# Kernel tuning notes

Hardware: AMD Instinct MI355X
Metric: run time of the kernel (lower is better)

The kernel has to match this reference:

```python
import jax, jax.numpy as jnp
import numpy as np

EPS = 1e-6


def _phi(x):
    # feature map: ELU(x) + 1, strictly positive
    return jax.nn.elu(x) + 1.0


def setup_inputs() -> dict:
    key = jax.random.key(0)
    kq, kk, kv, km, kz = jax.random.split(key, 5)
    B, H, T, D = 2, 32, 4096, 128
    Q = jax.random.normal(kq, (B, H, T, D), dtype=jnp.float32)
    K = jax.random.normal(kk, (B, H, T, D), dtype=jnp.float32)
    V = jax.random.normal(kv, (B, H, T, D), dtype=jnp.float32)
    M = jax.random.normal(km, (H, D, D), dtype=jnp.float32)
    z = jax.random.uniform(kz, (H, D), dtype=jnp.float32)
    return {"Q": Q, "K": K, "V": V, "M": M, "z": z}


def reference(Q, K, V, M, z):
    # ---- retrieve(Q) ----
    phi_Q = _phi(Q)                                   # (b,h,t,d)
    retrieved = jnp.einsum('bhtd,hde->bhte', phi_Q, M)
    norm = jnp.einsum('bhtd,hd->bht', phi_Q, z)[..., None]
    out = retrieved / jnp.maximum(norm, EPS)          # (b,h,t,d)

    # ---- update(K, V): detached (stop_gradient) running accumulation ----
    phi_K_b = _phi(jax.lax.stop_gradient(K)).mean(0)  # (h,t,d)
    V_b = jax.lax.stop_gradient(V).mean(0)            # (h,t,d)
    M_new = M + jnp.einsum('htd,hte->hde', phi_K_b, V_b)
    z_new = z + phi_K_b.sum(1)
    return out, M_new, z_new
```

## Files before the change

### kernel.cpp

```cpp
#include <hip/hip_runtime.h>
#include <cstdint>
#include <cstddef>


typedef __bf16 bf16x8 __attribute__((ext_vector_type(8)));
typedef float  f32x4  __attribute__((ext_vector_type(4)));
typedef unsigned short us8v __attribute__((ext_vector_type(8)));

#define NB 2
#define NH 32
#define NT 4096
#define ND 128
#define NC 8
#define TCH (NT / NC)
#define NUPD (NH * NC)
#define NOUT (NB * NH * (NT / 128))
#define EPSF 1e-6f

__device__ __forceinline__ float phi_f(float x) {
    return x > 0.0f ? x + 1.0f : __expf(x);
}

__device__ __forceinline__ unsigned short f2bf(float f) {
    union { float f; unsigned u; } c; c.f = f;
    unsigned r = c.u + 0x7FFFu + ((c.u >> 16) & 1u);
    return (unsigned short)(r >> 16);
}

__device__ __forceinline__ bf16x8 pack8(float a0, float a1, float a2, float a3,
                                        float a4, float a5, float a6, float a7) {
    union { us8v u; bf16x8 h; } r;
    r.u[0] = f2bf(a0); r.u[1] = f2bf(a1); r.u[2] = f2bf(a2); r.u[3] = f2bf(a3);
    r.u[4] = f2bf(a4); r.u[5] = f2bf(a5); r.u[6] = f2bf(a6); r.u[7] = f2bf(a7);
    return r.h;
}

__global__ __launch_bounds__(256) void k_prep(const float* __restrict__ M,
                                              unsigned short* __restrict__ Mt) {
    int idx = blockIdx.x * 256 + threadIdx.x;
    int h = idx >> 14, rem = idx & 16383;
    int e = rem >> 7, d = rem & 127;
    Mt[idx] = f2bf(M[(h << 14) + (d << 7) + e]);
}

__device__ __forceinline__ void upd_body(int blk, const float* __restrict__ K,
                                         const float* __restrict__ V,
                                         float* __restrict__ part,
                                         float* __restrict__ zpart,
                                         unsigned short* smem, float* zacc) {
    const int tid = threadIdx.x;
    const int h = blk >> 3, ch = blk & 7;
    unsigned short* Kl = smem;
    unsigned short* Vl = smem + 8192;

    const size_t bstr = (size_t)NH * NT * ND;
    const float* K0 = K + (size_t)h * NT * ND + (size_t)ch * TCH * ND;
    const float* K1 = K0 + bstr;
    const float* V0 = V + (size_t)h * NT * ND + (size_t)ch * TCH * ND;
    const float* V1 = V0 + bstr;
    if (tid < 128) zacc[tid] = 0.0f;

    const int L = tid & 31, d0 = L << 2, tb = tid >> 5;
    const int lane = tid & 63, wave = tid >> 6;
    const int mw = (wave & 1) << 6, nw = (wave >> 1) << 6;
    const int l15 = lane & 15, qd = lane >> 4;
    const int grp = tb ^ (L & 7);

    float zp0 = 0.f, zp1 = 0.f, zp2 = 0.f, zp3 = 0.f;
    f32x4 acc[4][4];
#pragma unroll
    for (int a = 0; a < 4; ++a)
#pragma unroll
        for (int b = 0; b < 4; ++b) acc[a][b] = (f32x4){0.f, 0.f, 0.f, 0.f};

    for (int st = 0; st < TCH / 64; ++st) {
        us8v kpu[4], vpu[4];
#pragma unroll
        for (int i = 0; i < 8; ++i) {
            size_t off = ((size_t)(st * 64 + tb * 8 + i)) * ND + d0;
            float4 a0 = *(const float4*)(K0 + off);
            float4 a1 = *(const float4*)(K1 + off);
            float4 b0 = *(const float4*)(V0 + off);
            float4 b1 = *(const float4*)(V1 + off);
            float p0 = 0.5f * (phi_f(a0.x) + phi_f(a1.x));
            float p1 = 0.5f * (phi_f(a0.y) + phi_f(a1.y));
            float p2 = 0.5f * (phi_f(a0.z) + phi_f(a1.z));
            float p3 = 0.5f * (phi_f(a0.w) + phi_f(a1.w));
            zp0 += p0; zp1 += p1; zp2 += p2; zp3 += p3;
            kpu[0][i] = f2bf(p0); kpu[1][i] = f2bf(p1);
            kpu[2][i] = f2bf(p2); kpu[3][i] = f2bf(p3);
            vpu[0][i] = f2bf(0.5f * (b0.x + b1.x));
            vpu[1][i] = f2bf(0.5f * (b0.y + b1.y));
            vpu[2][i] = f2bf(0.5f * (b0.z + b1.z));
            vpu[3][i] = f2bf(0.5f * (b0.w + b1.w));
        }
        __syncthreads();
#pragma unroll
        for (int j = 0; j < 4; ++j) {
            *(us8v*)&Kl[(d0 + j) * 64 + grp * 8] = kpu[j];
            *(us8v*)&Vl[(d0 + j) * 64 + grp * 8] = vpu[j];
        }
        __syncthreads();
#pragma unroll
        for (int kk = 0; kk < 2; ++kk) {
            bf16x8 af[4], bv[4];
#pragma unroll
            for (int im = 0; im < 4; ++im) {
                int d = mw + im * 16 + l15;
                int sg = (kk * 4 + qd) ^ ((d >> 2) & 7);
                af[im] = *(const bf16x8*)&Kl[d * 64 + sg * 8];
            }
#pragma unroll
            for (int in = 0; in < 4; ++in) {
                int e = nw + in * 16 + l15;
                int sg = (kk * 4 + qd) ^ ((e >> 2) & 7);
                bv[in] = *(const bf16x8*)&Vl[e * 64 + sg * 8];
            }
#pragma unroll
            for (int im = 0; im < 4; ++im)
#pragma unroll
                for (int in = 0; in < 4; ++in)
                    acc[im][in] = __builtin_amdgcn_mfma_f32_16x16x32_bf16(
                        af[im], bv[in], acc[im][in], 0, 0, 0);
        }
    }

    atomicAdd(&zacc[d0 + 0], zp0);
    atomicAdd(&zacc[d0 + 1], zp1);
    atomicAdd(&zacc[d0 + 2], zp2);
    atomicAdd(&zacc[d0 + 3], zp3);
    __syncthreads();
    if (tid < 128) zpart[((size_t)h * NC + ch) * 128 + tid] = zacc[tid];

    float* pb = part + ((size_t)h * NC + ch) * 16384;
#pragma unroll
    for (int im = 0; im < 4; ++im)
#pragma unroll
        for (int in = 0; in < 4; ++in) {
            int col = nw + in * 16 + l15;
#pragma unroll
            for (int rg = 0; rg < 4; ++rg) {
                int row = mw + im * 16 + qd * 4 + rg;
                pb[(size_t)row * ND + col] = acc[im][in][rg];
            }
        }
}

__device__ __forceinline__ void out_body(int blk, const float* __restrict__ Q,
                                         const unsigned short* __restrict__ Mt,
                                         const float* __restrict__ z,
                                         float* __restrict__ out,
                                         unsigned short* smem) {
    const int tid = threadIdx.x;
    const int tile = blk & 31, bh = blk >> 5, h = bh & 31;
    const float* Qb = Q + ((size_t)bh * NT + (size_t)tile * 128) * ND;
    unsigned short* Bs = smem;

    {
        const us8v* src = (const us8v*)(Mt + (size_t)h * 16384);
#pragma unroll
        for (int i = 0; i < 8; ++i) {
            int idx = i * 256 + tid;
            int e = idx >> 4, d8 = idx & 15;
            *(us8v*)&Bs[e * 136 + d8 * 8] = src[idx];
        }
    }
    const int lane = tid & 63, wave = tid >> 6;
    const int mw = (wave & 1) << 6, nw = (wave >> 1) << 6;
    const int l15 = lane & 15, qd = lane >> 4;

    bf16x8 zf[4];
#pragma unroll
    for (int kk = 0; kk < 4; ++kk) {
        const float* zp = z + h * ND + kk * 32 + qd * 8;
        float4 z0 = *(const float4*)zp;
        float4 z1 = *(const float4*)(zp + 4);
        zf[kk] = pack8(z0.x, z0.y, z0.z, z0.w, z1.x, z1.y, z1.z, z1.w);
    }
    __syncthreads();

    f32x4 acc[4][4], accN[4];
#pragma unroll
    for (int a = 0; a < 4; ++a) {
        accN[a] = (f32x4){0.f, 0.f, 0.f, 0.f};
#pragma unroll
        for (int b = 0; b < 4; ++b) acc[a][b] = (f32x4){0.f, 0.f, 0.f, 0.f};
    }

#pragma unroll
    for (int im = 0; im < 4; ++im) {
        int row = mw + im * 16 + l15;
        const float* qr = Qb + (size_t)row * ND;
        bf16x8 af[4];
#pragma unroll
        for (int kk = 0; kk < 4; ++kk) {
            const float* qp = qr + kk * 32 + qd * 8;
            float4 q0 = *(const float4*)qp;
            float4 q1 = *(const float4*)(qp + 4);
            af[kk] = pack8(phi_f(q0.x), phi_f(q0.y), phi_f(q0.z), phi_f(q0.w),
                           phi_f(q1.x), phi_f(q1.y), phi_f(q1.z), phi_f(q1.w));
        }
#pragma unroll
        for (int kk = 0; kk < 4; ++kk)
            accN[im] = __builtin_amdgcn_mfma_f32_16x16x32_bf16(
                af[kk], zf[kk], accN[im], 0, 0, 0);
#pragma unroll
        for (int in = 0; in < 4; ++in) {
            int e = nw + in * 16 + l15;
#pragma unroll
            for (int kk = 0; kk < 4; ++kk) {
                bf16x8 bv = *(const bf16x8*)&Bs[e * 136 + kk * 32 + qd * 8];
                acc[im][in] = __builtin_amdgcn_mfma_f32_16x16x32_bf16(
                    af[kk], bv, acc[im][in], 0, 0, 0);
            }
        }
    }

    float* outb = out + ((size_t)bh * NT + (size_t)tile * 128) * ND;
#pragma unroll
    for (int im = 0; im < 4; ++im) {
#pragma unroll
        for (int rg = 0; rg < 4; ++rg) {
            float inv = 1.0f / fmaxf(accN[im][rg], EPSF);
            int row = mw + im * 16 + qd * 4 + rg;
#pragma unroll
            for (int in = 0; in < 4; ++in) {
                int col = nw + in * 16 + l15;
                outb[(size_t)row * ND + col] = acc[im][in][rg] * inv;
            }
        }
    }
}

__global__ __launch_bounds__(256) void k_main(const float* __restrict__ Q,
                                              const float* __restrict__ K,
                                              const float* __restrict__ V,
                                              const unsigned short* __restrict__ Mt,
                                              const float* __restrict__ z,
                                              float* __restrict__ out,
                                              float* __restrict__ part,
                                              float* __restrict__ zpart) {
    __shared__ unsigned short smem[128 * 136];
    __shared__ float zacc[128];
    if (blockIdx.x < NUPD)
        upd_body(blockIdx.x, K, V, part, zpart, smem, zacc);
    else
        out_body(blockIdx.x - NUPD, Q, Mt, z, out, smem);
}

__global__ __launch_bounds__(256) void k_reduce(const float* __restrict__ M,
                                                const float* __restrict__ z,
                                                const float* __restrict__ part,
                                                const float* __restrict__ zpart,
                                                float* __restrict__ outM,
                                                float* __restrict__ outz) {
    int idx = blockIdx.x * 256 + threadIdx.x;
    int h = idx >> 14, de = idx & 16383;
    float s = M[idx];
    const float* p = part + (size_t)h * NC * 16384 + de;
#pragma unroll
    for (int c = 0; c < NC; ++c) s += p[(size_t)c * 16384];
    outM[idx] = s;
    if (idx < NH * ND) {
        int hh = idx >> 7, d = idx & 127;
        float sz = z[idx];
        const float* pz = zpart + (size_t)hh * NC * 128 + d;
#pragma unroll
        for (int c = 0; c < NC; ++c) sz += pz[c * 128];
        outz[idx] = sz;
    }
}

extern "C" void kernel_launch(void* const* d_in, const int* in_sizes, int n_in,
                              void* d_out, int out_size, void* d_ws, size_t ws_size,
                              hipStream_t stream) {
    const float* Q = (const float*)d_in[0];
    const float* K = (const float*)d_in[1];
    const float* V = (const float*)d_in[2];
    const float* M = (const float*)d_in[3];
    const float* z = (const float*)d_in[4];

    float* out0 = (float*)d_out;
    float* outM = out0 + (size_t)NB * NH * NT * ND;
    float* outz = outM + (size_t)NH * ND * ND;

    unsigned short* Mt = (unsigned short*)d_ws;
    float* part  = (float*)((char*)d_ws + (1u << 20));
    float* zpart = part + (size_t)NH * NC * ND * ND;

    k_prep<<<2048, 256, 0, stream>>>(M, Mt);
    k_main<<<NUPD + NOUT, 256, 0, stream>>>(Q, K, V, Mt, z, out0, part, zpart);
    k_reduce<<<(NH * ND * ND) / 256, 256, 0, stream>>>(M, z, part, zpart, outM, outz);
}
```

Baseline: 424.0 us.

## Use native bf16 conversion, swizzled LDS, smaller shared memory and occupancy hint

Replaces the manual round-to-nearest-even bf16 packing with native __bf16 casts, which can map to hardware conversion instructions. Moves the 0.5 and 0.25 mean scales out of the inner loop and applies them at the partial-sum stores. Replaces the padded 136-stride LDS layout for M with an XOR-swizzled 128-stride layout and reuses that buffer for the z accumulator. Adds a launch_bounds hint of 4 blocks per CU and uses the hardware reciprocal for normalisation. The native casts and the fast reciprocal may round differently from the old code, and the occupancy hint may increase register spills.

```diff
diff --git a/kernel.cpp b/kernel.cpp
--- a/kernel.cpp
+++ b/kernel.cpp
@@ -21,18 +21,26 @@
     return x > 0.0f ? x + 1.0f : __expf(x);
 }
 
-__device__ __forceinline__ unsigned short f2bf(float f) {
-    union { float f; unsigned u; } c; c.f = f;
-    unsigned r = c.u + 0x7FFFu + ((c.u >> 16) & 1u);
-    return (unsigned short)(r >> 16);
-}
-
-__device__ __forceinline__ bf16x8 pack8(float a0, float a1, float a2, float a3,
-                                        float a4, float a5, float a6, float a7) {
-    union { us8v u; bf16x8 h; } r;
-    r.u[0] = f2bf(a0); r.u[1] = f2bf(a1); r.u[2] = f2bf(a2); r.u[3] = f2bf(a3);
-    r.u[4] = f2bf(a4); r.u[5] = f2bf(a5); r.u[6] = f2bf(a6); r.u[7] = f2bf(a7);
-    return r.h;
+__device__ __forceinline__ unsigned short f2bfn(float f) {
+    union { __bf16 h; unsigned short u; } c;
+    c.h = (__bf16)f;
+    return c.u;
+}
+
+__device__ __forceinline__ bf16x8 cvt8(float4 a, float4 b) {
+    bf16x8 r;
+    r[0] = (__bf16)a.x; r[1] = (__bf16)a.y; r[2] = (__bf16)a.z; r[3] = (__bf16)a.w;
+    r[4] = (__bf16)b.x; r[5] = (__bf16)b.y; r[6] = (__bf16)b.z; r[7] = (__bf16)b.w;
+    return r;
+}
+
+__device__ __forceinline__ bf16x8 cvt8phi(float4 a, float4 b) {
+    bf16x8 r;
+    r[0] = (__bf16)phi_f(a.x); r[1] = (__bf16)phi_f(a.y);
+    r[2] = (__bf16)phi_f(a.z); r[3] = (__bf16)phi_f(a.w);
+    r[4] = (__bf16)phi_f(b.x); r[5] = (__bf16)phi_f(b.y);
+    r[6] = (__bf16)phi_f(b.z); r[7] = (__bf16)phi_f(b.w);
+    return r;
 }
 
 __global__ __launch_bounds__(256) void k_prep(const float* __restrict__ M,
@@ -40,14 +48,14 @@
     int idx = blockIdx.x * 256 + threadIdx.x;
     int h = idx >> 14, rem = idx & 16383;
     int e = rem >> 7, d = rem & 127;
-    Mt[idx] = f2bf(M[(h << 14) + (d << 7) + e]);
+    Mt[idx] = f2bfn(M[(h << 14) + (d << 7) + e]);
 }
 
 __device__ __forceinline__ void upd_body(int blk, const float* __restrict__ K,
                                          const float* __restrict__ V,
                                          float* __restrict__ part,
                                          float* __restrict__ zpart,
-                                         unsigned short* smem, float* zacc) {
+                                         unsigned short* smem) {
     const int tid = threadIdx.x;
     const int h = blk >> 3, ch = blk & 7;
     unsigned short* Kl = smem;
@@ -58,7 +66,6 @@
     const float* K1 = K0 + bstr;
     const float* V0 = V + (size_t)h * NT * ND + (size_t)ch * TCH * ND;
     const float* V1 = V0 + bstr;
-    if (tid < 128) zacc[tid] = 0.0f;
 
     const int L = tid & 31, d0 = L << 2, tb = tid >> 5;
     const int lane = tid & 63, wave = tid >> 6;
@@ -74,7 +81,7 @@
         for (int b = 0; b < 4; ++b) acc[a][b] = (f32x4){0.f, 0.f, 0.f, 0.f};
 
     for (int st = 0; st < TCH / 64; ++st) {
-        us8v kpu[4], vpu[4];
+        bf16x8 kpu[4], vpu[4];
 #pragma unroll
         for (int i = 0; i < 8; ++i) {
             size_t off = ((size_t)(st * 64 + tb * 8 + i)) * ND + d0;
@@ -82,23 +89,23 @@
             float4 a1 = *(const float4*)(K1 + off);
             float4 b0 = *(const float4*)(V0 + off);
             float4 b1 = *(const float4*)(V1 + off);
-            float p0 = 0.5f * (phi_f(a0.x) + phi_f(a1.x));
-            float p1 = 0.5f * (phi_f(a0.y) + phi_f(a1.y));
-            float p2 = 0.5f * (phi_f(a0.z) + phi_f(a1.z));
-            float p3 = 0.5f * (phi_f(a0.w) + phi_f(a1.w));
+            float p0 = phi_f(a0.x) + phi_f(a1.x);
+            float p1 = phi_f(a0.y) + phi_f(a1.y);
+            float p2 = phi_f(a0.z) + phi_f(a1.z);
+            float p3 = phi_f(a0.w) + phi_f(a1.w);
             zp0 += p0; zp1 += p1; zp2 += p2; zp3 += p3;
-            kpu[0][i] = f2bf(p0); kpu[1][i] = f2bf(p1);
-            kpu[2][i] = f2bf(p2); kpu[3][i] = f2bf(p3);
-            vpu[0][i] = f2bf(0.5f * (b0.x + b1.x));
-            vpu[1][i] = f2bf(0.5f * (b0.y + b1.y));
-            vpu[2][i] = f2bf(0.5f * (b0.z + b1.z));
-            vpu[3][i] = f2bf(0.5f * (b0.w + b1.w));
+            kpu[0][i] = (__bf16)p0; kpu[1][i] = (__bf16)p1;
+            kpu[2][i] = (__bf16)p2; kpu[3][i] = (__bf16)p3;
+            vpu[0][i] = (__bf16)(b0.x + b1.x);
+            vpu[1][i] = (__bf16)(b0.y + b1.y);
+            vpu[2][i] = (__bf16)(b0.z + b1.z);
+            vpu[3][i] = (__bf16)(b0.w + b1.w);
         }
         __syncthreads();
 #pragma unroll
         for (int j = 0; j < 4; ++j) {
-            *(us8v*)&Kl[(d0 + j) * 64 + grp * 8] = kpu[j];
-            *(us8v*)&Vl[(d0 + j) * 64 + grp * 8] = vpu[j];
+            *(bf16x8*)&Kl[(d0 + j) * 64 + grp * 8] = kpu[j];
+            *(bf16x8*)&Vl[(d0 + j) * 64 + grp * 8] = vpu[j];
         }
         __syncthreads();
 #pragma unroll
@@ -125,12 +132,16 @@
         }
     }
 
+    __syncthreads();
+    float* zacc = (float*)smem;
+    if (tid < 128) zacc[tid] = 0.0f;
+    __syncthreads();
     atomicAdd(&zacc[d0 + 0], zp0);
     atomicAdd(&zacc[d0 + 1], zp1);
     atomicAdd(&zacc[d0 + 2], zp2);
     atomicAdd(&zacc[d0 + 3], zp3);
     __syncthreads();
-    if (tid < 128) zpart[((size_t)h * NC + ch) * 128 + tid] = zacc[tid];
+    if (tid < 128) zpart[((size_t)h * NC + ch) * 128 + tid] = 0.5f * zacc[tid];
 
     float* pb = part + ((size_t)h * NC + ch) * 16384;
 #pragma unroll
@@ -141,7 +152,7 @@
 #pragma unroll
             for (int rg = 0; rg < 4; ++rg) {
                 int row = mw + im * 16 + qd * 4 + rg;
-                pb[(size_t)row * ND + col] = acc[im][in][rg];
+                pb[(size_t)row * ND + col] = 0.25f * acc[im][in][rg];
             }
         }
 }
@@ -162,20 +173,19 @@
         for (int i = 0; i < 8; ++i) {
             int idx = i * 256 + tid;
             int e = idx >> 4, d8 = idx & 15;
-            *(us8v*)&Bs[e * 136 + d8 * 8] = src[idx];
+            *(us8v*)&Bs[e * 128 + ((d8 ^ (e & 7)) << 3)] = src[idx];
         }
     }
     const int lane = tid & 63, wave = tid >> 6;
     const int mw = (wave & 1) << 6, nw = (wave >> 1) << 6;
     const int l15 = lane & 15, qd = lane >> 4;
+    const int s7 = l15 & 7;
 
     bf16x8 zf[4];
 #pragma unroll
     for (int kk = 0; kk < 4; ++kk) {
         const float* zp = z + h * ND + kk * 32 + qd * 8;
-        float4 z0 = *(const float4*)zp;
-        float4 z1 = *(const float4*)(zp + 4);
-        zf[kk] = pack8(z0.x, z0.y, z0.z, z0.w, z1.x, z1.y, z1.z, z1.w);
+        zf[kk] = cvt8(*(const float4*)zp, *(const float4*)(zp + 4));
     }
     __syncthreads();
 
@@ -195,10 +205,7 @@
 #pragma unroll
         for (int kk = 0; kk < 4; ++kk) {
             const float* qp = qr + kk * 32 + qd * 8;
-            float4 q0 = *(const float4*)qp;
-            float4 q1 = *(const float4*)(qp + 4);
-            af[kk] = pack8(phi_f(q0.x), phi_f(q0.y), phi_f(q0.z), phi_f(q0.w),
-                           phi_f(q1.x), phi_f(q1.y), phi_f(q1.z), phi_f(q1.w));
+            af[kk] = cvt8phi(*(const float4*)qp, *(const float4*)(qp + 4));
         }
 #pragma unroll
         for (int kk = 0; kk < 4; ++kk)
@@ -209,7 +216,7 @@
             int e = nw + in * 16 + l15;
 #pragma unroll
             for (int kk = 0; kk < 4; ++kk) {
-                bf16x8 bv = *(const bf16x8*)&Bs[e * 136 + kk * 32 + qd * 8];
+                bf16x8 bv = *(const bf16x8*)&Bs[e * 128 + ((((kk << 2) | qd) ^ s7) << 3)];
                 acc[im][in] = __builtin_amdgcn_mfma_f32_16x16x32_bf16(
                     af[kk], bv, acc[im][in], 0, 0, 0);
             }
@@ -221,7 +228,7 @@
     for (int im = 0; im < 4; ++im) {
 #pragma unroll
         for (int rg = 0; rg < 4; ++rg) {
-            float inv = 1.0f / fmaxf(accN[im][rg], EPSF);
+            float inv = __builtin_amdgcn_rcpf(fmaxf(accN[im][rg], EPSF));
             int row = mw + im * 16 + qd * 4 + rg;
 #pragma unroll
             for (int in = 0; in < 4; ++in) {
@@ -232,18 +239,17 @@
     }
 }
 
-__global__ __launch_bounds__(256) void k_main(const float* __restrict__ Q,
-                                              const float* __restrict__ K,
-                                              const float* __restrict__ V,
-                                              const unsigned short* __restrict__ Mt,
-                                              const float* __restrict__ z,
-                                              float* __restrict__ out,
-                                              float* __restrict__ part,
-                                              float* __restrict__ zpart) {
-    __shared__ unsigned short smem[128 * 136];
-    __shared__ float zacc[128];
+__global__ __launch_bounds__(256, 4) void k_main(const float* __restrict__ Q,
+                                                 const float* __restrict__ K,
+                                                 const float* __restrict__ V,
+                                                 const unsigned short* __restrict__ Mt,
+                                                 const float* __restrict__ z,
+                                                 float* __restrict__ out,
+                                                 float* __restrict__ part,
+                                                 float* __restrict__ zpart) {
+    __shared__ unsigned short smem[128 * 128];
     if (blockIdx.x < NUPD)
-        upd_body(blockIdx.x, K, V, part, zpart, smem, zacc);
+        upd_body(blockIdx.x, K, V, part, zpart, smem);
     else
         out_body(blockIdx.x - NUPD, Q, Mt, z, out, smem);
 }
```

After: 530.9 us. 1.25x slower.
